# Kernel tuning notes

Measured on AMD Instinct MI355X. Metric: run time of the kernel, lower is better.

Reference implementation:

```python
import jax, jax.numpy as jnp
import numpy as np

K = 2            # number of attention heads (k in __init__)
NEG = -9.0e15    # mask fill value from the torch code
N, C, CO = 6144, 128, 128


def _ln(x, g, b, eps=1e-5):
    m = x.mean(-1, keepdims=True)
    v = ((x - m) ** 2).mean(-1, keepdims=True)
    return (x - m) / jnp.sqrt(v + eps) * g + b


def setup_inputs() -> dict:
    key = jax.random.key(0)
    ks = jax.random.split(key, 6)
    x = jax.random.normal(ks[0], (N, C), jnp.float32)
    adj = (jax.random.uniform(ks[1], (N, N)) < 0.01).astype(jnp.float32)
    ff0_w = jax.random.normal(ks[2], (K, C, C), jnp.float32) / np.float32(np.sqrt(C))
    ff1_w = jax.random.normal(ks[3], (K, CO, C), jnp.float32) / np.float32(np.sqrt(C))
    attn_w = jax.random.normal(ks[4], (K, 2 * C), jnp.float32) / np.float32(np.sqrt(2 * C))
    return dict(
        x=x, adj=adj, ff0_w=ff0_w, ff1_w=ff1_w, attn_w=attn_w,
        g1=jnp.ones((C,), jnp.float32), b1=jnp.zeros((C,), jnp.float32),
        g2=jnp.ones((C,), jnp.float32), b2=jnp.zeros((C,), jnp.float32),
    )


def reference(x, adj, ff0_w, ff1_w, attn_w, g1, b1, g2, b2):
    n, c = x.shape
    co = ff1_w.shape[1]
    x_norm = _ln(x, g1, b1)
    # torch does adj = adj + eye(n) each iteration; since adj >= 0 the mask
    # (adj > 0) is identical for every iteration: original edges plus self-loops.
    mask = (adj > 0) | jnp.eye(n, dtype=bool)
    h_next = jnp.zeros((n, co), x.dtype)
    for i in range(K):  # small fixed head count, structurally distinct weights
        h = x_norm @ ff0_w[i].T  # [n, c]
        # attn_fc(cat(h_i, h_j)) == a1.h_i + a2.h_j  (exact decomposition of
        # the concat+linear; avoids materializing the [n, n, 2c] tensor)
        s_src = h @ attn_w[i, :c]  # [n], contribution of row node i
        s_dst = h @ attn_w[i, c:]  # [n], contribution of col node j
        e = jax.nn.leaky_relu(s_src[:, None] + s_dst[None, :])  # [n, n]
        e = jnp.where(mask, e, jnp.float32(NEG))
        atten = jax.nn.softmax(e, axis=1)  # dropout p=0.0 -> identity
        att = atten @ h + x  # residual adds pre-norm x
        att = _ln(att, g2, b2)
        h_next = h_next + jax.nn.elu(att @ ff1_w[i].T) / K
    return h_next
```

## Files before the change

### kernel.cpp

```cpp
#include <hip/hip_runtime.h>
#include <math.h>

#define Nn 6144
#define Cc 128
#define NHD 2
#define MAXDEG 1024

__device__ __forceinline__ float wave_red_sum(float v) {
#pragma unroll
  for (int o = 32; o; o >>= 1) v += __shfl_xor(v, o);
  return v;
}

template <bool IS_MAX>
__device__ __forceinline__ void block_red2(float& a, float& b, float* red) {
#pragma unroll
  for (int o = 32; o; o >>= 1) {
    float ta = __shfl_xor(a, o), tb = __shfl_xor(b, o);
    if (IS_MAX) { a = fmaxf(a, ta); b = fmaxf(b, tb); }
    else        { a += ta;          b += tb;          }
  }
  int wid = threadIdx.x >> 6;
  __syncthreads();
  if ((threadIdx.x & 63) == 0) { red[wid] = a; red[4 + wid] = b; }
  __syncthreads();
  if (IS_MAX) {
    a = fmaxf(fmaxf(red[0], red[1]), fmaxf(red[2], red[3]));
    b = fmaxf(fmaxf(red[4], red[5]), fmaxf(red[6], red[7]));
  } else {
    a = red[0] + red[1] + red[2] + red[3];
    b = red[4] + red[5] + red[6] + red[7];
  }
}

__global__ __launch_bounds__(256) void k_ff0_fused(
    const float* __restrict__ x, const float* __restrict__ g1,
    const float* __restrict__ b1, const float* __restrict__ Bw,
    const float* __restrict__ aw, float* __restrict__ h,
    float* __restrict__ ssrc, float* __restrict__ sdst) {
  __shared__ float Axn[128][36];
  __shared__ float Bs[64][132];
  const int t = threadIdx.x;
  const int head = blockIdx.y;
  const int row0 = blockIdx.x * 32;
  const float* Bh = Bw + (size_t)head * Cc * Cc;

  {
    const int row = t >> 3, seg = t & 7;
    const int cb = seg * 16;
    const float* xr = x + (size_t)(row0 + row) * Cc + cb;
    float v[16], gg[16], bb[16];
#pragma unroll
    for (int i = 0; i < 16; i += 4) {
      float4 t4 = *(const float4*)(xr + i);
      v[i] = t4.x; v[i + 1] = t4.y; v[i + 2] = t4.z; v[i + 3] = t4.w;
      float4 g4 = *(const float4*)(g1 + cb + i);
      gg[i] = g4.x; gg[i + 1] = g4.y; gg[i + 2] = g4.z; gg[i + 3] = g4.w;
      float4 b4 = *(const float4*)(b1 + cb + i);
      bb[i] = b4.x; bb[i + 1] = b4.y; bb[i + 2] = b4.z; bb[i + 3] = b4.w;
    }
    float s = 0.f;
#pragma unroll
    for (int i = 0; i < 16; i++) s += v[i];
    s += __shfl_xor(s, 1); s += __shfl_xor(s, 2); s += __shfl_xor(s, 4);
    float mean = s * (1.0f / 128.0f);
    float q = 0.f;
#pragma unroll
    for (int i = 0; i < 16; i++) { float d_ = v[i] - mean; q += d_ * d_; }
    q += __shfl_xor(q, 1); q += __shfl_xor(q, 2); q += __shfl_xor(q, 4);
    float rstd = rsqrtf(q * (1.0f / 128.0f) + 1e-5f);
#pragma unroll
    for (int i = 0; i < 16; i++)
      Axn[cb + i][row] = (v[i] - mean) * rstd * gg[i] + bb[i];
  }
  __syncthreads();

  const int tr = t & 7, tc = t >> 3;
  float acc[4][4];
#pragma unroll
  for (int i = 0; i < 4; i++)
#pragma unroll
    for (int j = 0; j < 4; j++) acc[i][j] = 0.f;

  for (int kt = 0; kt < Cc; kt += 64) {
    for (int i = t; i < 2048; i += 256) {
      int cc2 = i >> 4, k4 = i & 15;
      float4 v = *(const float4*)(Bh + (size_t)cc2 * Cc + kt + k4 * 4);
      Bs[k4 * 4 + 0][cc2] = v.x; Bs[k4 * 4 + 1][cc2] = v.y;
      Bs[k4 * 4 + 2][cc2] = v.z; Bs[k4 * 4 + 3][cc2] = v.w;
    }
    __syncthreads();
#pragma unroll
    for (int k = 0; k < 64; k++) {
      float4 a4 = *(const float4*)&Axn[kt + k][tr * 4];
      float4 b4 = *(const float4*)&Bs[k][tc * 4];
      float av[4] = {a4.x, a4.y, a4.z, a4.w};
      float bv[4] = {b4.x, b4.y, b4.z, b4.w};
#pragma unroll
      for (int i = 0; i < 4; i++)
#pragma unroll
        for (int j = 0; j < 4; j++) acc[i][j] = fmaf(av[i], bv[j], acc[i][j]);
    }
    __syncthreads();
  }

  float psrc[4], pdst[4];
  {
    float4 w1 = *(const float4*)(aw + head * 2 * Cc + tc * 4);
    float4 w2 = *(const float4*)(aw + head * 2 * Cc + Cc + tc * 4);
#pragma unroll
    for (int i = 0; i < 4; i++) {
      float* op = h + ((size_t)head * Nn + row0 + tr * 4 + i) * Cc + tc * 4;
      *(float4*)op = make_float4(acc[i][0], acc[i][1], acc[i][2], acc[i][3]);
      psrc[i] = acc[i][0] * w1.x + acc[i][1] * w1.y + acc[i][2] * w1.z + acc[i][3] * w1.w;
      pdst[i] = acc[i][0] * w2.x + acc[i][1] * w2.y + acc[i][2] * w2.z + acc[i][3] * w2.w;
    }
  }
  float* epart = &Bs[0][0];
#pragma unroll
  for (int i = 0; i < 4; i++) {
    epart[((tc * 32) + (tr * 4 + i)) * 2 + 0] = psrc[i];
    epart[((tc * 32) + (tr * 4 + i)) * 2 + 1] = pdst[i];
  }
  __syncthreads();
  if (t < 64) {
    int row = t >> 1, s = t & 1;
    float v = 0.f;
#pragma unroll
    for (int g = 0; g < 32; g++) v += epart[(g * 32 + row) * 2 + s];
    (s ? sdst : ssrc)[head * Nn + row0 + row] = v;
  }
}

__global__ __launch_bounds__(256) void k_ff1_comb(const float* __restrict__ A,
                                                  const float* __restrict__ Bw,
                                                  float* __restrict__ out) {
  __shared__ float As[64][36];
  __shared__ float Bs[64][132];
  const int t = threadIdx.x;
  const int row0 = blockIdx.x * 32;
  const int tr = t & 7, tc = t >> 3;
  float sum[4][4];
#pragma unroll
  for (int i = 0; i < 4; i++)
#pragma unroll
    for (int j = 0; j < 4; j++) sum[i][j] = 0.f;

  for (int head = 0; head < NHD; head++) {
    const float* Ah = A + (size_t)head * Nn * Cc;
    const float* Bh = Bw + (size_t)head * Cc * Cc;
    float acc[4][4];
#pragma unroll
    for (int i = 0; i < 4; i++)
#pragma unroll
      for (int j = 0; j < 4; j++) acc[i][j] = 0.f;

    for (int kt = 0; kt < Cc; kt += 64) {
      __syncthreads();
      for (int i = t; i < 512; i += 256) {
        int rr = i >> 4, k4 = i & 15;
        float4 v = *(const float4*)(Ah + (size_t)(row0 + rr) * Cc + kt + k4 * 4);
        As[k4 * 4 + 0][rr] = v.x; As[k4 * 4 + 1][rr] = v.y;
        As[k4 * 4 + 2][rr] = v.z; As[k4 * 4 + 3][rr] = v.w;
      }
      for (int i = t; i < 2048; i += 256) {
        int cc2 = i >> 4, k4 = i & 15;
        float4 v = *(const float4*)(Bh + (size_t)cc2 * Cc + kt + k4 * 4);
        Bs[k4 * 4 + 0][cc2] = v.x; Bs[k4 * 4 + 1][cc2] = v.y;
        Bs[k4 * 4 + 2][cc2] = v.z; Bs[k4 * 4 + 3][cc2] = v.w;
      }
      __syncthreads();
#pragma unroll
      for (int k = 0; k < 64; k++) {
        float4 a4 = *(const float4*)&As[k][tr * 4];
        float4 b4 = *(const float4*)&Bs[k][tc * 4];
        float av[4] = {a4.x, a4.y, a4.z, a4.w};
        float bv[4] = {b4.x, b4.y, b4.z, b4.w};
#pragma unroll
        for (int i = 0; i < 4; i++)
#pragma unroll
          for (int j = 0; j < 4; j++) acc[i][j] = fmaf(av[i], bv[j], acc[i][j]);
      }
    }
#pragma unroll
    for (int i = 0; i < 4; i++)
#pragma unroll
      for (int j = 0; j < 4; j++) {
        float v = acc[i][j];
        v = (v > 0.f) ? v : (expf(v) - 1.f);
        sum[i][j] = fmaf(v, 0.5f, sum[i][j]);
      }
  }
#pragma unroll
  for (int i = 0; i < 4; i++) {
    float* op = out + (size_t)(row0 + tr * 4 + i) * Cc + tc * 4;
    *(float4*)op = make_float4(sum[i][0], sum[i][1], sum[i][2], sum[i][3]);
  }
}

__global__ __launch_bounds__(256) void k_attn(
    const float* __restrict__ adj, const float* __restrict__ x,
    const float* __restrict__ h, const float* __restrict__ ssrc,
    const float* __restrict__ sdst, const float* __restrict__ g2,
    const float* __restrict__ b2, float* __restrict__ att_out) {
  __shared__ __align__(16) int nbr[MAXDEG];
  __shared__ __align__(16) float wts[NHD][MAXDEG];
  __shared__ float red[8];
  __shared__ int cnt;
  const int t = threadIdx.x;
  const int r = blockIdx.x;
  if (t == 0) cnt = 0;
  __syncthreads();
  const float4* arow = (const float4*)(adj + (size_t)r * Nn);
  for (int i = t; i < Nn / 4; i += 256) {
    float4 v = arow[i];
    int j = i * 4;
    if (v.x > 0.f || j + 0 == r) { int p = atomicAdd(&cnt, 1); if (p < MAXDEG) nbr[p] = j + 0; }
    if (v.y > 0.f || j + 1 == r) { int p = atomicAdd(&cnt, 1); if (p < MAXDEG) nbr[p] = j + 1; }
    if (v.z > 0.f || j + 2 == r) { int p = atomicAdd(&cnt, 1); if (p < MAXDEG) nbr[p] = j + 2; }
    if (v.w > 0.f || j + 3 == r) { int p = atomicAdd(&cnt, 1); if (p < MAXDEG) nbr[p] = j + 3; }
  }
  __syncthreads();
  const int deg = min(cnt, MAXDEG);
  const float s0 = ssrc[r], s1 = ssrc[Nn + r];
  float m0 = -3.0e38f, m1 = -3.0e38f;
  for (int k = t; k < deg; k += 256) {
    int j = nbr[k];
    float e0 = s0 + sdst[j];
    float e1 = s1 + sdst[Nn + j];
    e0 = (e0 > 0.f) ? e0 : 0.01f * e0;
    e1 = (e1 > 0.f) ? e1 : 0.01f * e1;
    wts[0][k] = e0; wts[1][k] = e1;
    m0 = fmaxf(m0, e0); m1 = fmaxf(m1, e1);
  }
  block_red2<true>(m0, m1, red);
  float l0 = 0.f, l1 = 0.f;
  for (int k = t; k < deg; k += 256) {
    float w0 = __expf(wts[0][k] - m0); wts[0][k] = w0; l0 += w0;
    float w1 = __expf(wts[1][k] - m1); wts[1][k] = w1; l1 += w1;
  }
  block_red2<false>(l0, l1, red);
  {
    const int hd = t >> 7, g = (t >> 5) & 3, c4 = t & 31;
    const float* hp = h + (size_t)hd * Nn * Cc + c4 * 4;
    float4 a4 = make_float4(0.f, 0.f, 0.f, 0.f);
#pragma unroll 2
    for (int k = g; k < deg; k += 4) {
      float w = wts[hd][k];
      const float4 hv = *(const float4*)(hp + (size_t)nbr[k] * Cc);
      a4.x = fmaf(w, hv.x, a4.x);
      a4.y = fmaf(w, hv.y, a4.y);
      a4.z = fmaf(w, hv.z, a4.z);
      a4.w = fmaf(w, hv.w, a4.w);
    }
    __syncthreads();
    float4* part = (float4*)&wts[0][0];
    part[t] = a4;
    __syncthreads();
    float* attbuf = (float*)nbr;
    if (t < 64) {
      const int hd2 = t >> 5, cb = t & 31;
      float4 p0 = part[hd2 * 128 + 0  + cb];
      float4 p1 = part[hd2 * 128 + 32 + cb];
      float4 p2 = part[hd2 * 128 + 64 + cb];
      float4 p3 = part[hd2 * 128 + 96 + cb];
      float sx_ = p0.x + p1.x + p2.x + p3.x;
      float sy_ = p0.y + p1.y + p2.y + p3.y;
      float sz_ = p0.z + p1.z + p2.z + p3.z;
      float sw_ = p0.w + p1.w + p2.w + p3.w;
      const float inv2 = 1.0f / (hd2 ? l1 : l0);
      const float4 xv = *(const float4*)(x + (size_t)r * Cc + cb * 4);
      float4 att4;
      att4.x = fmaf(sx_, inv2, xv.x);
      att4.y = fmaf(sy_, inv2, xv.y);
      att4.z = fmaf(sz_, inv2, xv.z);
      att4.w = fmaf(sw_, inv2, xv.w);
      ((float4*)attbuf)[hd2 * 32 + cb] = att4;
    }
    __syncthreads();
    const int c = t & 127;
    float att = attbuf[(t >> 7) * 128 + c];
    float s = wave_red_sum(att);
    int wid = t >> 6;
    __syncthreads();
    if ((t & 63) == 0) red[wid] = s;
    __syncthreads();
    float mean = (red[(t >> 7) * 2] + red[(t >> 7) * 2 + 1]) * (1.0f / Cc);
    float d = att - mean;
    float q = wave_red_sum(d * d);
    __syncthreads();
    if ((t & 63) == 0) red[wid] = q;
    __syncthreads();
    float var = (red[(t >> 7) * 2] + red[(t >> 7) * 2 + 1]) * (1.0f / Cc);
    float rstd = rsqrtf(var + 1e-5f);
    att_out[((size_t)(t >> 7) * Nn + r) * Cc + c] = d * rstd * g2[c] + b2[c];
  }
}

extern "C" void kernel_launch(void* const* d_in, const int* in_sizes, int n_in,
                              void* d_out, int out_size, void* d_ws, size_t ws_size,
                              hipStream_t stream) {
  const float* x   = (const float*)d_in[0];
  const float* adj = (const float*)d_in[1];
  const float* ff0 = (const float*)d_in[2];
  const float* ff1 = (const float*)d_in[3];
  const float* aw  = (const float*)d_in[4];
  const float* g1  = (const float*)d_in[5];
  const float* b1  = (const float*)d_in[6];
  const float* g2  = (const float*)d_in[7];
  const float* b2  = (const float*)d_in[8];
  float* out = (float*)d_out;

  float* ws   = (float*)d_ws;
  float* h    = ws;
  float* ssrc = h + (size_t)2 * Nn * Cc;
  float* sdst = ssrc + 2 * Nn;
  float* attn = sdst + 2 * Nn;

  hipLaunchKernelGGL(k_ff0_fused, dim3(Nn / 32, NHD), dim3(256), 0, stream,
                     x, g1, b1, ff0, aw, h, ssrc, sdst);
  hipLaunchKernelGGL(k_attn, dim3(Nn), dim3(256), 0, stream, adj, x, h, ssrc, sdst, g2, b2, attn);
  hipLaunchKernelGGL(k_ff1_comb, dim3(Nn / 32), dim3(256), 0, stream, attn, ff1, out);
}
```

Measured before the change: 295.1 us.

## Fuse ff1 projection, ELU and head averaging into attention kernel

Removes the separate tiled ff1 GEMM kernel and instead computes each row's ff1 matvec inside the per-row attention block, after the second layer norm. This drops the round trip of the [2,N,C] attention buffer through global memory and one kernel launch. In exchange, each block reads a full 128x128 weight row slice per head from global or L2 without shared-memory reuse across rows, so weight traffic rises sharply and the matvec adds a serial 128-long dot product per thread.

```diff
diff --git a/kernel.cpp b/kernel.cpp
--- a/kernel.cpp
+++ b/kernel.cpp
@@ -132,77 +132,12 @@
   }
 }
 
-__global__ __launch_bounds__(256) void k_ff1_comb(const float* __restrict__ A,
-                                                  const float* __restrict__ Bw,
-                                                  float* __restrict__ out) {
-  __shared__ float As[64][36];
-  __shared__ float Bs[64][132];
-  const int t = threadIdx.x;
-  const int row0 = blockIdx.x * 32;
-  const int tr = t & 7, tc = t >> 3;
-  float sum[4][4];
-#pragma unroll
-  for (int i = 0; i < 4; i++)
-#pragma unroll
-    for (int j = 0; j < 4; j++) sum[i][j] = 0.f;
-
-  for (int head = 0; head < NHD; head++) {
-    const float* Ah = A + (size_t)head * Nn * Cc;
-    const float* Bh = Bw + (size_t)head * Cc * Cc;
-    float acc[4][4];
-#pragma unroll
-    for (int i = 0; i < 4; i++)
-#pragma unroll
-      for (int j = 0; j < 4; j++) acc[i][j] = 0.f;
-
-    for (int kt = 0; kt < Cc; kt += 64) {
-      __syncthreads();
-      for (int i = t; i < 512; i += 256) {
-        int rr = i >> 4, k4 = i & 15;
-        float4 v = *(const float4*)(Ah + (size_t)(row0 + rr) * Cc + kt + k4 * 4);
-        As[k4 * 4 + 0][rr] = v.x; As[k4 * 4 + 1][rr] = v.y;
-        As[k4 * 4 + 2][rr] = v.z; As[k4 * 4 + 3][rr] = v.w;
-      }
-      for (int i = t; i < 2048; i += 256) {
-        int cc2 = i >> 4, k4 = i & 15;
-        float4 v = *(const float4*)(Bh + (size_t)cc2 * Cc + kt + k4 * 4);
-        Bs[k4 * 4 + 0][cc2] = v.x; Bs[k4 * 4 + 1][cc2] = v.y;
-        Bs[k4 * 4 + 2][cc2] = v.z; Bs[k4 * 4 + 3][cc2] = v.w;
-      }
-      __syncthreads();
-#pragma unroll
-      for (int k = 0; k < 64; k++) {
-        float4 a4 = *(const float4*)&As[k][tr * 4];
-        float4 b4 = *(const float4*)&Bs[k][tc * 4];
-        float av[4] = {a4.x, a4.y, a4.z, a4.w};
-        float bv[4] = {b4.x, b4.y, b4.z, b4.w};
-#pragma unroll
-        for (int i = 0; i < 4; i++)
-#pragma unroll
-          for (int j = 0; j < 4; j++) acc[i][j] = fmaf(av[i], bv[j], acc[i][j]);
-      }
-    }
-#pragma unroll
-    for (int i = 0; i < 4; i++)
-#pragma unroll
-      for (int j = 0; j < 4; j++) {
-        float v = acc[i][j];
-        v = (v > 0.f) ? v : (expf(v) - 1.f);
-        sum[i][j] = fmaf(v, 0.5f, sum[i][j]);
-      }
-  }
-#pragma unroll
-  for (int i = 0; i < 4; i++) {
-    float* op = out + (size_t)(row0 + tr * 4 + i) * Cc + tc * 4;
-    *(float4*)op = make_float4(sum[i][0], sum[i][1], sum[i][2], sum[i][3]);
-  }
-}
-
-__global__ __launch_bounds__(256) void k_attn(
+__global__ __launch_bounds__(256) void k_attn_ff1(
     const float* __restrict__ adj, const float* __restrict__ x,
     const float* __restrict__ h, const float* __restrict__ ssrc,
     const float* __restrict__ sdst, const float* __restrict__ g2,
-    const float* __restrict__ b2, float* __restrict__ att_out) {
+    const float* __restrict__ b2, const float* __restrict__ ff1,
+    float* __restrict__ out) {
   __shared__ __align__(16) int nbr[MAXDEG];
   __shared__ __align__(16) float wts[NHD][MAXDEG];
   __shared__ float red[8];
@@ -240,6 +175,7 @@
     float w1 = __expf(wts[1][k] - m1); wts[1][k] = w1; l1 += w1;
   }
   block_red2<false>(l0, l1, red);
+  float att;
   {
     const int hd = t >> 7, g = (t >> 5) & 3, c4 = t & 31;
     const float* hp = h + (size_t)hd * Nn * Cc + c4 * 4;
@@ -278,22 +214,43 @@
       ((float4*)attbuf)[hd2 * 32 + cb] = att4;
     }
     __syncthreads();
-    const int c = t & 127;
-    float att = attbuf[(t >> 7) * 128 + c];
+    att = ((float*)nbr)[(t >> 7) * 128 + (t & 127)];
+  }
+  const int hd = t >> 7, c = t & 127;
+  float* lnbuf = (float*)&wts[0][0];
+  {
     float s = wave_red_sum(att);
     int wid = t >> 6;
     __syncthreads();
     if ((t & 63) == 0) red[wid] = s;
     __syncthreads();
-    float mean = (red[(t >> 7) * 2] + red[(t >> 7) * 2 + 1]) * (1.0f / Cc);
+    float mean = (red[hd * 2] + red[hd * 2 + 1]) * (1.0f / Cc);
     float d = att - mean;
     float q = wave_red_sum(d * d);
     __syncthreads();
     if ((t & 63) == 0) red[wid] = q;
     __syncthreads();
-    float var = (red[(t >> 7) * 2] + red[(t >> 7) * 2 + 1]) * (1.0f / Cc);
+    float var = (red[hd * 2] + red[hd * 2 + 1]) * (1.0f / Cc);
     float rstd = rsqrtf(var + 1e-5f);
-    att_out[((size_t)(t >> 7) * Nn + r) * Cc + c] = d * rstd * g2[c] + b2[c];
+    lnbuf[t] = d * rstd * g2[c] + b2[c];
+  }
+  __syncthreads();
+  {
+    const float* wrow = ff1 + ((size_t)hd * Cc + c) * Cc;
+    const float4* ln4 = (const float4*)(lnbuf + hd * 128);
+    float acc = 0.f;
+#pragma unroll 8
+    for (int k4 = 0; k4 < 32; k4++) {
+      float4 w4 = *(const float4*)(wrow + k4 * 4);
+      float4 a4 = ln4[k4];
+      acc += a4.x * w4.x + a4.y * w4.y + a4.z * w4.z + a4.w * w4.w;
+    }
+    acc = (acc > 0.f) ? acc : (expf(acc) - 1.f);
+    acc *= 0.5f;
+    float* combuf = (float*)nbr;
+    combuf[t] = acc;
+    __syncthreads();
+    if (t < 128) out[(size_t)r * Cc + t] = combuf[t] + combuf[128 + t];
   }
 }
 
@@ -315,10 +272,9 @@
   float* h    = ws;
   float* ssrc = h + (size_t)2 * Nn * Cc;
   float* sdst = ssrc + 2 * Nn;
-  float* attn = sdst + 2 * Nn;
 
   hipLaunchKernelGGL(k_ff0_fused, dim3(Nn / 32, NHD), dim3(256), 0, stream,
                      x, g1, b1, ff0, aw, h, ssrc, sdst);
-  hipLaunchKernelGGL(k_attn, dim3(Nn), dim3(256), 0, stream, adj, x, h, ssrc, sdst, g2, b2, attn);
-  hipLaunchKernelGGL(k_ff1_comb, dim3(Nn / 32), dim3(256), 0, stream, attn, ff1, out);
-}
+  hipLaunchKernelGGL(k_attn_ff1, dim3(Nn), dim3(256), 0, stream,
+                     adj, x, h, ssrc, sdst, g2, b2, ff1, out);
+}
```

Result: slower. 335.1 us (+13.6%).
